# Performance work log

Measured on AMD Instinct MI355X. Metric: run time of the kernel, lower is better.

## Reference

```python
import jax, jax.numpy as jnp
import numpy as np

N = 100_000       # nodes
F = 128           # feature dim (== num_inputs)
DEG = 16          # in-degree per node
E = N * DEG       # edges
OUT = 128         # num_outputs


def setup_inputs() -> dict:
    key = jax.random.key(0)
    k1, k2, k3, k4 = jax.random.split(key, 4)
    node_feat_input = jax.random.normal(k1, (N, F), dtype=jnp.float32)
    # col 0: destination (index_add target). tile(arange) guarantees degree == DEG > 0.
    dst = jnp.tile(jnp.arange(N, dtype=jnp.int64), DEG)
    src = jax.random.randint(k2, (E,), 0, N, dtype=jnp.int64)
    adjacency_input = jnp.stack([dst, src], axis=1)  # [E, 2]
    indices = jnp.arange(N, dtype=jnp.int64)  # unused by forward, kept for signature parity
    # Xavier-uniform init matching SparseGCN.initialize (fan_in = 2*F, fan_out = OUT)
    bound = float(np.sqrt(6.0 / (2 * F + OUT)))
    weight = jax.random.uniform(k3, (2 * F, OUT), dtype=jnp.float32, minval=-bound, maxval=bound)
    bias = jax.random.uniform(k4, (OUT,), dtype=jnp.float32, minval=-bound, maxval=bound)
    return {
        "node_feat_input": node_feat_input,
        "adjacency_input": adjacency_input,
        "indices": indices,
        "weight": weight,
        "bias": bias,
    }


def reference(node_feat_input, adjacency_input, indices, weight, bias):
    n = node_feat_input.shape[0]
    dst = adjacency_input[:, 0]
    src = adjacency_input[:, 1]
    # scatter-sum of gathered neighbor features (index_add_ equivalent)
    sum_neighbors = jax.ops.segment_sum(node_feat_input[src], dst, num_segments=n)
    degree = jax.ops.segment_sum(
        jnp.ones_like(dst, dtype=node_feat_input.dtype), dst, num_segments=n
    )
    # diag(1/degree) @ sum_neighbors == elementwise row scaling
    h_neigh = sum_neighbors / degree[:, None]
    temp = jnp.concatenate([node_feat_input, h_neigh], axis=1) @ weight + bias
    return jax.nn.sigmoid(temp)
```

## Files before the change

### kernel.cpp

```cpp
#include <hip/hip_runtime.h>
#include <hip/hip_bf16.h>

#define NN 100000
#define FF 128
#define DEG 16
#define OUTC 128

typedef __attribute__((ext_vector_type(8))) short short8;
typedef __attribute__((ext_vector_type(4))) float float4v;

__device__ __forceinline__ unsigned short f2b(float f) {
    union { float f; unsigned u; } v; v.f = f;
    unsigned r = v.u + 0x7fff + ((v.u >> 16) & 1);
    return (unsigned short)(r >> 16);
}
__device__ __forceinline__ float b2f(unsigned bits16) {
    union { unsigned u; float f; } v; v.u = bits16 << 16; return v.f;
}

__global__ __launch_bounds__(256) void prep_x(const float4* __restrict__ x,
                                              uint2* __restrict__ xb) {
    int t = blockIdx.x * 256 + threadIdx.x;
    float4 v = x[t];
    uint2 o;
    o.x = (unsigned)f2b(v.x) | ((unsigned)f2b(v.y) << 16);
    o.y = (unsigned)f2b(v.z) | ((unsigned)f2b(v.w) << 16);
    xb[t] = o;
}

__global__ __launch_bounds__(256) void prep_w(const float* __restrict__ w,
                                              unsigned short* __restrict__ wp) {
    int t = blockIdx.x * 256 + threadIdx.x;
    int j = t & 7, lane = (t >> 3) & 63, kk = (t >> 9) & 7, ct = t >> 12;
    int k = kk * 32 + (lane >> 4) * 8 + j;
    int c = ct * 16 + (lane & 15);
    wp[t] = f2b(w[k * 128 + c]);
}

__global__ __launch_bounds__(256) void gather_k(const unsigned* __restrict__ xb,
                                                const int* __restrict__ adj,
                                                unsigned* __restrict__ hb) {
    int node = (int)((blockIdx.x * 256 + threadIdx.x) >> 6);
    int lane = threadIdx.x & 63;
    if (node >= NN) return;
    float a0 = 0.f, a1 = 0.f;
#pragma unroll
    for (int k = 0; k < DEG; ++k) {
        int s = adj[2 * (node + k * NN) + 1];
        unsigned v = xb[(size_t)s * 64 + lane];
        a0 += b2f(v & 0xffffu);
        a1 += b2f(v >> 16);
    }
    a0 *= (1.f / 16.f); a1 *= (1.f / 16.f);
    hb[(size_t)node * 64 + lane] = (unsigned)f2b(a0) | ((unsigned)f2b(a1) << 16);
}

#define GEMM_BLOCKS 1024
#define WAVES_PER_HALF 2048
__global__ __launch_bounds__(256, 2) void gemm_k(const unsigned short* __restrict__ xb,
                                                 const unsigned short* __restrict__ hb,
                                                 const unsigned short* __restrict__ wp,
                                                 const float* __restrict__ bias,
                                                 float* __restrict__ out) {
    const int wv = blockIdx.x * 4 + (threadIdx.x >> 6);
    const int lane = threadIdx.x & 63;
    const int half = wv & 1;
    const int wslot = wv >> 1;

    short8 bfrag[4][8];
    const short8* wpv = (const short8*)wp;
#pragma unroll
    for (int j = 0; j < 4; ++j) {
        int ct = half * 4 + j;
#pragma unroll
        for (int kk = 0; kk < 8; ++kk)
            bfrag[j][kk] = wpv[(ct * 8 + kk) * 64 + lane];
    }
    float bval[4];
#pragma unroll
    for (int j = 0; j < 4; ++j)
        bval[j] = bias[(half * 4 + j) * 16 + (lane & 15)];

    const int arow = lane & 15;
    const int kg = lane >> 4;

    for (int s = wslot; s < NN / 16; s += WAVES_PER_HALF) {
        int node = s * 16 + arow;
        const short8* xrow = (const short8*)(xb + (size_t)node * 128) + kg;
        const short8* hrow = (const short8*)(hb + (size_t)node * 128) + kg;

        float4v acc[4];
#pragma unroll
        for (int j = 0; j < 4; ++j) acc[j] = (float4v){0.f, 0.f, 0.f, 0.f};

#pragma unroll
        for (int kk = 0; kk < 8; ++kk) {
            short8 afrag = (kk < 4) ? xrow[kk * 4] : hrow[(kk - 4) * 4];
#pragma unroll
            for (int j = 0; j < 4; ++j)
                acc[j] = __builtin_amdgcn_mfma_f32_16x16x32_bf16(afrag, bfrag[j][kk], acc[j], 0, 0, 0);
        }
#pragma unroll
        for (int j = 0; j < 4; ++j) {
            int col = (half * 4 + j) * 16 + (lane & 15);
#pragma unroll
            for (int r = 0; r < 4; ++r) {
                float v = acc[j][r] + bval[j];
                v = 1.f / (1.f + __expf(-v));
                out[(size_t)(s * 16 + kg * 4 + r) * 128 + col] = v;
            }
        }
    }
}

extern "C" void kernel_launch(void* const* d_in, const int* in_sizes, int n_in,
                              void* d_out, int out_size, void* d_ws, size_t ws_size,
                              hipStream_t stream) {
    const float* x    = (const float*)d_in[0];
    const int*   adj  = (const int*)d_in[1];
    const float* w    = (const float*)d_in[3];
    const float* bias = (const float*)d_in[4];
    float* out = (float*)d_out;

    unsigned short* xb = (unsigned short*)d_ws;
    unsigned short* hb = (unsigned short*)((char*)d_ws + 25600000);
    unsigned short* wp = (unsigned short*)((char*)d_ws + 51200000);

    prep_x<<<12500, 256, 0, stream>>>((const float4*)x, (uint2*)xb);
    prep_w<<<128, 256, 0, stream>>>(w, wp);
    gather_k<<<25000, 256, 0, stream>>>((const unsigned*)xb, adj, (unsigned*)hb);
    gemm_k<<<GEMM_BLOCKS, 256, 0, stream>>>(xb, hb, wp, bias, out);
}
```

Baseline: 190.1 us.

## Fuse neighbor gather into GEMM kernel via LDS-staged aggregated features

Merges the gather/mean kernel and the MFMA GEMM kernel into one kernel. Each block handles two 16-node strips: waves compute the neighbor means for their rows into shared memory, synchronize, then run the bf16 MFMA GEMM reading x from global and h from LDS. This removes the write and re-read of the intermediate h buffer and one kernel launch. In exchange each block must reload the full weight fragments into registers for a single strip, and the gather's latency is no longer spread across a persistent GEMM loop.

```diff
diff --git a/kernel.cpp b/kernel.cpp
--- a/kernel.cpp
+++ b/kernel.cpp
@@ -5,6 +5,7 @@
 #define FF 128
 #define DEG 16
 #define OUTC 128
+#define NSTRIPS 6250
 
 typedef __attribute__((ext_vector_type(8))) short short8;
 typedef __attribute__((ext_vector_type(4))) float float4v;
@@ -37,78 +38,79 @@
     wp[t] = f2b(w[k * 128 + c]);
 }
 
-__global__ __launch_bounds__(256) void gather_k(const unsigned* __restrict__ xb,
-                                                const int* __restrict__ adj,
-                                                unsigned* __restrict__ hb) {
-    int node = (int)((blockIdx.x * 256 + threadIdx.x) >> 6);
-    int lane = threadIdx.x & 63;
-    if (node >= NN) return;
-    float a0 = 0.f, a1 = 0.f;
-#pragma unroll
-    for (int k = 0; k < DEG; ++k) {
-        int s = adj[2 * (node + k * NN) + 1];
-        unsigned v = xb[(size_t)s * 64 + lane];
-        a0 += b2f(v & 0xffffu);
-        a1 += b2f(v >> 16);
-    }
-    a0 *= (1.f / 16.f); a1 *= (1.f / 16.f);
-    hb[(size_t)node * 64 + lane] = (unsigned)f2b(a0) | ((unsigned)f2b(a1) << 16);
-}
+__global__ __launch_bounds__(256, 2) void fused_k(const unsigned* __restrict__ xb32,
+                                                  const int* __restrict__ adj,
+                                                  const unsigned short* __restrict__ wp,
+                                                  const float* __restrict__ bias,
+                                                  float* __restrict__ out) {
+    __shared__ unsigned hlds[2][16][68];
 
-#define GEMM_BLOCKS 1024
-#define WAVES_PER_HALF 2048
-__global__ __launch_bounds__(256, 2) void gemm_k(const unsigned short* __restrict__ xb,
-                                                 const unsigned short* __restrict__ hb,
-                                                 const unsigned short* __restrict__ wp,
-                                                 const float* __restrict__ bias,
-                                                 float* __restrict__ out) {
-    const int wv = blockIdx.x * 4 + (threadIdx.x >> 6);
+    const int wv   = threadIdx.x >> 6;
     const int lane = threadIdx.x & 63;
+    const int sloc = wv >> 1;
     const int half = wv & 1;
-    const int wslot = wv >> 1;
+    const int strip = blockIdx.x * 2 + sloc;
 
     short8 bfrag[4][8];
     const short8* wpv = (const short8*)wp;
 #pragma unroll
-    for (int j = 0; j < 4; ++j) {
-        int ct = half * 4 + j;
+    for (int j = 0; j < 4; ++j)
 #pragma unroll
         for (int kk = 0; kk < 8; ++kk)
-            bfrag[j][kk] = wpv[(ct * 8 + kk) * 64 + lane];
-    }
+            bfrag[j][kk] = wpv[((half * 4 + j) * 8 + kk) * 64 + lane];
     float bval[4];
 #pragma unroll
     for (int j = 0; j < 4; ++j)
         bval[j] = bias[(half * 4 + j) * 16 + (lane & 15)];
 
+#pragma unroll 2
+    for (int r = 0; r < 8; ++r) {
+        int node = strip * 16 + half * 8 + r;
+        float a0 = 0.f, a1 = 0.f;
+#pragma unroll
+        for (int k = 0; k < DEG; ++k) {
+            int s = adj[2 * (node + k * NN) + 1];
+            unsigned v = xb32[(size_t)s * 64 + lane];
+            a0 += b2f(v & 0xffffu);
+            a1 += b2f(v >> 16);
+        }
+        a0 *= (1.f / 16.f); a1 *= (1.f / 16.f);
+        hlds[sloc][half * 8 + r][lane] = (unsigned)f2b(a0) | ((unsigned)f2b(a1) << 16);
+    }
+    __syncthreads();
+
     const int arow = lane & 15;
-    const int kg = lane >> 4;
+    const int kg   = lane >> 4;
+    const int node = strip * 16 + arow;
+    const short8* xchunk = (const short8*)xb32 + (size_t)node * 16 + kg;
 
-    for (int s = wslot; s < NN / 16; s += WAVES_PER_HALF) {
-        int node = s * 16 + arow;
-        const short8* xrow = (const short8*)(xb + (size_t)node * 128) + kg;
-        const short8* hrow = (const short8*)(hb + (size_t)node * 128) + kg;
-
-        float4v acc[4];
+    float4v acc[4];
 #pragma unroll
-        for (int j = 0; j < 4; ++j) acc[j] = (float4v){0.f, 0.f, 0.f, 0.f};
+    for (int j = 0; j < 4; ++j) acc[j] = (float4v){0.f, 0.f, 0.f, 0.f};
 
 #pragma unroll
-        for (int kk = 0; kk < 8; ++kk) {
-            short8 afrag = (kk < 4) ? xrow[kk * 4] : hrow[(kk - 4) * 4];
+    for (int kk = 0; kk < 4; ++kk) {
+        short8 afrag = xchunk[kk * 4];
 #pragma unroll
-            for (int j = 0; j < 4; ++j)
-                acc[j] = __builtin_amdgcn_mfma_f32_16x16x32_bf16(afrag, bfrag[j][kk], acc[j], 0, 0, 0);
-        }
+        for (int j = 0; j < 4; ++j)
+            acc[j] = __builtin_amdgcn_mfma_f32_16x16x32_bf16(afrag, bfrag[j][kk], acc[j], 0, 0, 0);
+    }
 #pragma unroll
-        for (int j = 0; j < 4; ++j) {
-            int col = (half * 4 + j) * 16 + (lane & 15);
+    for (int kk = 4; kk < 8; ++kk) {
+        short8 afrag = *(const short8*)&hlds[sloc][arow][(kg + 4 * (kk - 4)) * 4];
 #pragma unroll
-            for (int r = 0; r < 4; ++r) {
-                float v = acc[j][r] + bval[j];
-                v = 1.f / (1.f + __expf(-v));
-                out[(size_t)(s * 16 + kg * 4 + r) * 128 + col] = v;
-            }
+        for (int j = 0; j < 4; ++j)
+            acc[j] = __builtin_amdgcn_mfma_f32_16x16x32_bf16(afrag, bfrag[j][kk], acc[j], 0, 0, 0);
+    }
+
+#pragma unroll
+    for (int j = 0; j < 4; ++j) {
+        int col = (half * 4 + j) * 16 + (lane & 15);
+#pragma unroll
+        for (int r = 0; r < 4; ++r) {
+            float v = acc[j][r] + bval[j];
+            v = 1.f / (1.f + __expf(-v));
+            out[(size_t)(strip * 16 + kg * 4 + r) * 128 + col] = v;
         }
     }
 }
@@ -123,11 +125,9 @@
     float* out = (float*)d_out;
 
     unsigned short* xb = (unsigned short*)d_ws;
-    unsigned short* hb = (unsigned short*)((char*)d_ws + 25600000);
-    unsigned short* wp = (unsigned short*)((char*)d_ws + 51200000);
+    unsigned short* wp = (unsigned short*)((char*)d_ws + 25600000);
 
     prep_x<<<12500, 256, 0, stream>>>((const float4*)x, (uint2*)xb);
     prep_w<<<128, 256, 0, stream>>>(w, wp);
-    gather_k<<<25000, 256, 0, stream>>>((const unsigned*)xb, adj, (unsigned*)hb);
-    gemm_k<<<GEMM_BLOCKS, 256, 0, stream>>>(xb, hb, wp, bias, out);
+    fused_k<<<NSTRIPS / 2, 256, 0, stream>>>((const unsigned*)xb, adj, wp, bias, out);
 }
```

After: 314.8 us. 1.66x slower.

## Stage full weight in LDS and compute all output columns per wave

Applied to the files above, without the earlier changes.

Before, each wave held half of the packed bf16 weight in registers and covered half the output columns, so every 16-row strip's A fragments were loaded from global memory by two waves. Now each block copies the whole packed weight (64 KB) into shared memory, and each wave computes all 128 output columns for its strip, loading A fragments once. The grid is halved. This trades fewer global A loads and less register pressure for per-MFMA LDS reads of B fragments, plus a 64 KB LDS footprint that may limit blocks per CU.

```diff
diff --git a/kernel.cpp b/kernel.cpp
--- a/kernel.cpp
+++ b/kernel.cpp
@@ -5,6 +5,7 @@
 #define FF 128
 #define DEG 16
 #define OUTC 128
+#define NSTRIPS 6250
 
 typedef __attribute__((ext_vector_type(8))) short short8;
 typedef __attribute__((ext_vector_type(4))) float float4v;
@@ -55,54 +56,59 @@
     hb[(size_t)node * 64 + lane] = (unsigned)f2b(a0) | ((unsigned)f2b(a1) << 16);
 }
 
-#define GEMM_BLOCKS 1024
-#define WAVES_PER_HALF 2048
+#define GEMM_BLOCKS 512
+#define GEMM_WAVES (GEMM_BLOCKS * 4)
 __global__ __launch_bounds__(256, 2) void gemm_k(const unsigned short* __restrict__ xb,
                                                  const unsigned short* __restrict__ hb,
                                                  const unsigned short* __restrict__ wp,
                                                  const float* __restrict__ bias,
                                                  float* __restrict__ out) {
+    __shared__ __align__(16) unsigned short wlds[32768];
+
+    {
+        const uint4* s4 = (const uint4*)wp;
+        uint4* d4 = (uint4*)wlds;
+#pragma unroll
+        for (int i = 0; i < 16; ++i)
+            d4[i * 256 + threadIdx.x] = s4[i * 256 + threadIdx.x];
+    }
+    __syncthreads();
+
     const int wv = blockIdx.x * 4 + (threadIdx.x >> 6);
     const int lane = threadIdx.x & 63;
-    const int half = wv & 1;
-    const int wslot = wv >> 1;
-
-    short8 bfrag[4][8];
-    const short8* wpv = (const short8*)wp;
-#pragma unroll
-    for (int j = 0; j < 4; ++j) {
-        int ct = half * 4 + j;
-#pragma unroll
-        for (int kk = 0; kk < 8; ++kk)
-            bfrag[j][kk] = wpv[(ct * 8 + kk) * 64 + lane];
-    }
-    float bval[4];
-#pragma unroll
-    for (int j = 0; j < 4; ++j)
-        bval[j] = bias[(half * 4 + j) * 16 + (lane & 15)];
-
     const int arow = lane & 15;
     const int kg = lane >> 4;
 
-    for (int s = wslot; s < NN / 16; s += WAVES_PER_HALF) {
-        int node = s * 16 + arow;
-        const short8* xrow = (const short8*)(xb + (size_t)node * 128) + kg;
-        const short8* hrow = (const short8*)(hb + (size_t)node * 128) + kg;
+    float bval[8];
+#pragma unroll
+    for (int j = 0; j < 8; ++j) bval[j] = bias[j * 16 + (lane & 15)];
 
-        float4v acc[4];
+    for (int s = wv; s < NSTRIPS; s += GEMM_WAVES) {
+        const int node = s * 16 + arow;
+        const short8* xrow = (const short8*)xb + (size_t)node * 16 + kg;
+        const short8* hrow = (const short8*)hb + (size_t)node * 16 + kg;
+
+        short8 afr[8];
 #pragma unroll
-        for (int j = 0; j < 4; ++j) acc[j] = (float4v){0.f, 0.f, 0.f, 0.f};
+        for (int kk = 0; kk < 4; ++kk) afr[kk] = xrow[kk * 4];
+#pragma unroll
+        for (int kk = 0; kk < 4; ++kk) afr[4 + kk] = hrow[kk * 4];
+
+        float4v acc[8];
+#pragma unroll
+        for (int j = 0; j < 8; ++j) acc[j] = (float4v){0.f, 0.f, 0.f, 0.f};
 
 #pragma unroll
-        for (int kk = 0; kk < 8; ++kk) {
-            short8 afrag = (kk < 4) ? xrow[kk * 4] : hrow[(kk - 4) * 4];
+        for (int kk = 0; kk < 8; ++kk)
 #pragma unroll
-            for (int j = 0; j < 4; ++j)
-                acc[j] = __builtin_amdgcn_mfma_f32_16x16x32_bf16(afrag, bfrag[j][kk], acc[j], 0, 0, 0);
-        }
+            for (int j = 0; j < 8; ++j) {
+                short8 bf = *(const short8*)&wlds[(((j * 8 + kk) * 64) + lane) * 8];
+                acc[j] = __builtin_amdgcn_mfma_f32_16x16x32_bf16(afr[kk], bf, acc[j], 0, 0, 0);
+            }
+
 #pragma unroll
-        for (int j = 0; j < 4; ++j) {
-            int col = (half * 4 + j) * 16 + (lane & 15);
+        for (int j = 0; j < 8; ++j) {
+            int col = j * 16 + (lane & 15);
 #pragma unroll
             for (int r = 0; r < 4; ++r) {
                 float v = acc[j][r] + bval[j];
```

Result: slower. 219.9 us (+15.7%).
